# Kernel tuning notes

Hardware: AMD Instinct MI355X
Metric: run time of the kernel (lower is better)

Reference implementation:

```python
import jax, jax.numpy as jnp
import numpy as np

EPS = 1e-5  # RMSNorm epsilon


def rmsnorm(x, w):
    return x * jax.lax.rsqrt(jnp.mean(x * x, axis=-1, keepdims=True) + EPS) * w


def mamba_forward(u, in_proj_w, conv_w, conv_b, x_proj_w, dt_proj_w, dt_proj_b,
                  A_log, D_param, mamba_out_w):
    # u: (b, L, dm) -- canonical Mamba block (expand=2, d_state=16, d_conv=4)
    b, L, dm = u.shape
    di, ds = A_log.shape
    dtr = dt_proj_w.shape[1]
    xz = jnp.einsum('bld,ed->ble', u, in_proj_w)          # (b,L,2*di)
    x_, z = jnp.split(xz, 2, axis=-1)                     # each (b,L,di)
    # causal depthwise conv over the sequence axis
    dconv = conv_w.shape[-1]
    xc = jnp.transpose(x_, (0, 2, 1))                     # (b,di,L)
    xc = jnp.pad(xc, ((0, 0), (0, 0), (dconv - 1, 0)))
    xc = jax.lax.conv_general_dilated(xc, conv_w, window_strides=(1,), padding='VALID',
                                      dimension_numbers=('NCH', 'OIH', 'NCH'),
                                      feature_group_count=di)
    xc = xc + conv_b[None, :, None]
    x_ = jax.nn.silu(jnp.transpose(xc, (0, 2, 1)))        # (b,L,di)
    # input-dependent dt, B, C
    x_dbl = jnp.einsum('bld,ed->ble', x_, x_proj_w)       # (b,L,dtr+2*ds)
    dt, B, C = jnp.split(x_dbl, [dtr, dtr + ds], axis=-1)
    delta = jax.nn.softplus(jnp.einsum('blr,dr->bld', dt, dt_proj_w) + dt_proj_b)  # (b,L,di)
    A = -jnp.exp(A_log)                                   # (di,ds)

    def step(h, inp):
        d_t, B_t, C_t, x_t = inp                          # (b,di),(b,ds),(b,ds),(b,di)
        dA = jnp.exp(d_t[:, :, None] * A)                 # (b,di,ds)
        h = dA * h + (d_t * x_t)[:, :, None] * B_t[:, None, :]
        y = jnp.einsum('bds,bs->bd', h, C_t)
        return h, y

    xs = (jnp.moveaxis(delta, 1, 0), jnp.moveaxis(B, 1, 0),
          jnp.moveaxis(C, 1, 0), jnp.moveaxis(x_, 1, 0))
    h0 = jnp.zeros((b, di, ds), dtype=u.dtype)
    _, ys = jax.lax.scan(step, h0, xs)                    # ys: (L,b,di)
    y = jnp.moveaxis(ys, 0, 1) + x_ * D_param             # (b,L,di)
    y = y * jax.nn.silu(z)
    return jnp.einsum('bld,od->blo', y, mamba_out_w)      # (b,L,dm)


def conv1x1(W, bvec, t):
    # t: (b, cin, L) -> (b, cout, L)
    return jnp.einsum('oi,bit->bot', W, t) + bvec[None, :, None]


def reference(x, w_norm1, w_norm2, W_ip, b_ip, W_fp, b_fp, W_wp, b_wp, W_op, b_op,
              in_proj_w, conv_w, conv_b, x_proj_w, dt_proj_w, dt_proj_b,
              A_log, D_param, mamba_out_w):
    # x: (b, L, D) -- module's (b, c, l) with l == input_dim = D, c == seq = L
    residual = x
    xn = rmsnorm(x, w_norm1)                 # RMSNorm over last (input_dim) axis
    xt = jnp.transpose(xn, (0, 2, 1))        # 'b c l -> b l c' : (b, D, L)
    ssm = conv1x1(W_ip, b_ip, xt)            # (b, 2D, L)
    ssm = conv1x1(W_fp, b_fp, ssm)           # (b, 2D, L)
    u = jnp.transpose(ssm, (0, 2, 1))        # (b, L, 2D): seq=L, d_model=2D
    m = mamba_forward(u, in_proj_w, conv_w, conv_b, x_proj_w, dt_proj_w, dt_proj_b,
                      A_log, D_param, mamba_out_w)
    m = rmsnorm(m, w_norm2) + u              # PostNormMamba residual
    ssm = jnp.transpose(m, (0, 2, 1))        # (b, 2D, L)
    w = conv1x1(W_wp, b_wp, xt)              # (b, 2D, L)
    w = w * jax.nn.sigmoid(w)                # swish
    out = conv1x1(W_op, b_op, w * ssm)       # (b, D, L)
    return jnp.transpose(out, (0, 2, 1)) + residual


def setup_inputs():
    key = jax.random.key(0)
    ks = jax.random.split(key, 16)
    D, L, b = 64, 4096, 4
    dm, di, ds, dconv = 2 * D, 4 * D, 16, 4
    dtr = (dm + 15) // 16  # dt_rank = ceil(d_model/16) = 8

    def n(k, shape, fan_in):
        return jax.random.normal(k, shape, jnp.float32) * (1.0 / np.sqrt(fan_in))

    return {
        'x': jax.random.normal(ks[0], (b, L, D), jnp.float32),
        'w_norm1': jnp.ones((D,), jnp.float32),
        'w_norm2': jnp.ones((dm,), jnp.float32),
        'W_ip': n(ks[1], (2 * D, D), D), 'b_ip': jnp.zeros((2 * D,), jnp.float32),
        'W_fp': n(ks[2], (2 * D, 2 * D), 2 * D), 'b_fp': jnp.zeros((2 * D,), jnp.float32),
        'W_wp': n(ks[3], (2 * D, D), D), 'b_wp': jnp.zeros((2 * D,), jnp.float32),
        'W_op': n(ks[4], (D, 2 * D), 2 * D), 'b_op': jnp.zeros((D,), jnp.float32),
        'in_proj_w': n(ks[5], (2 * di, dm), dm),
        'conv_w': n(ks[6], (di, 1, dconv), dconv),
        'conv_b': jnp.zeros((di,), jnp.float32),
        'x_proj_w': n(ks[7], (dtr + 2 * ds, di), di),
        'dt_proj_w': n(ks[8], (di, dtr), dtr),
        'dt_proj_b': jnp.full((di,), float(np.log(np.expm1(0.01))), jnp.float32),
        'A_log': jnp.log(jnp.broadcast_to(jnp.arange(1, ds + 1, dtype=jnp.float32), (di, ds))),
        'D_param': jnp.ones((di,), jnp.float32),
        'mamba_out_w': n(ks[9], (dm, di), di),
    }
```

## Files before the change

kernel.cpp:

```cpp
#include <hip/hip_runtime.h>
#include <hip/hip_bf16.h>

typedef __hip_bfloat16 bf16;
typedef __attribute__((ext_vector_type(8))) short bf16x8;
typedef __attribute__((ext_vector_type(4))) float f32x4;
#define DEV __device__ __forceinline__

constexpr int SEQ  = 4096;
constexpr int NB   = 4;
constexpr int NTOK = NB * SEQ;
constexpr float EPS = 1e-5f;
constexpr int NCH = 64;
constexpr int NCHUNK = SEQ / NCH;
constexpr float LOG2E = 1.44269504f;

constexpr int OFF_WDT  = 0;
constexpr int OFF_WB   = 2048;
constexpr int WB_IP = 0;
constexpr int WB_WP = 8192;
constexpr int WB_FP = 16384;
constexpr int WB_PR = 32768;
constexpr int WB_MO = 98304;
constexpr int WB_OP = 131072;
constexpr int WB_XP = 139264;
constexpr int WB_TOT = 151552;
constexpr int OFF_XDBL = OFF_WB + WB_TOT / 2;
constexpr int OFF_R1   = OFF_XDBL + NTOK * 40;
constexpr int OFF_WSW  = OFF_R1   + 1048576;
constexpr int OFF_U    = OFF_WSW  + 1048576;
constexpr int OFF_R2   = OFF_U    + 1048576;
constexpr int OFF_SILUZ= OFF_R2   + 2097152;
constexpr int OFF_XC   = OFF_SILUZ+ 2097152;
constexpr int OFF_G    = OFF_XC   + 2097152;
constexpr int OFF_FLAG = OFF_G    + 2097152;

DEV float b2f(bf16 x) { return __bfloat162float(x); }
DEV bf16 f2b(float x) { return __float2bfloat16(x); }
DEV short shof(bf16 h) { short s; __builtin_memcpy(&s, &h, 2); return s; }
DEV float ldin(const void* p, int i, int f) {
  return f ? ((const float*)p)[i] : b2f(((const bf16*)p)[i]);
}
DEV unsigned pack2(float a, float b) {
  bf16 ha = f2b(a), hb = f2b(b);
  unsigned short ua, ub;
  __builtin_memcpy(&ua, &ha, 2); __builtin_memcpy(&ub, &hb, 2);
  return (unsigned)ua | ((unsigned)ub << 16);
}
DEV float lo16f(unsigned u) { return __int_as_float((int)(u << 16)); }
DEV float hi16f(unsigned u) { return __int_as_float((int)(u & 0xffff0000u)); }
template<int CTRL>
DEV float dpp_add(float v) {
  int r = __builtin_amdgcn_update_dpp(0, __float_as_int(v), CTRL, 0xF, 0xF, false);
  return v + __int_as_float(r);
}
DEV float exp2f_fast(float a) { return __builtin_amdgcn_exp2f(a); }
DEV float softplus(float a) {
  return (a > 20.f) ? a : __logf(1.f + exp2f_fast(a * LOG2E));
}
DEV float silu(float a) { return a / (1.f + __expf(-a)); }

DEV void cpw(int e, int base, int count, const void* __restrict__ src,
             bf16* __restrict__ wb, int f) {
  int r = e - base;
  if (r >= 0 && r < count) wb[base + r] = f2b(ldin(src, r, f));
}
__global__ __launch_bounds__(256) void prep_k(
    const void* __restrict__ w_ip, const void* __restrict__ w_wp, const void* __restrict__ w_fp,
    const void* __restrict__ w_pr, const void* __restrict__ w_mo, const void* __restrict__ w_op,
    const void* __restrict__ w_x,  const void* __restrict__ w_dt,
    const void* __restrict__ x, float* __restrict__ wsf, int* __restrict__ flagp)
{
  __shared__ int cnt;
  if (threadIdx.x == 0) cnt = 0;
  __syncthreads();
  {
    float v = b2f(((const bf16*)x)[threadIdx.x]);
    int ok = (v == v) && fabsf(v) > 1e-4f && fabsf(v) < 100.f;
    atomicAdd(&cnt, ok);
  }
  __syncthreads();
  int f = (cnt > 204) ? 0 : 1;
  if (blockIdx.x == 0 && threadIdx.x == 0) *flagp = f;

  int e = blockIdx.x * 256 + threadIdx.x;
  bf16* wb = (bf16*)(wsf + OFF_WB);
  cpw(e, WB_IP, 8192,  w_ip, wb, f);
  cpw(e, WB_WP, 8192,  w_wp, wb, f);
  cpw(e, WB_FP, 16384, w_fp, wb, f);
  cpw(e, WB_PR, 65536, w_pr, wb, f);
  cpw(e, WB_MO, 32768, w_mo, wb, f);
  cpw(e, WB_OP, 8192,  w_op, wb, f);
  {
    int r = e - WB_XP;
    if (r >= 0 && r < 12288) wb[WB_XP + r] = (r < 10240) ? f2b(ldin(w_x, r, f)) : f2b(0.f);
  }
  if (e < 2048) {
    int r = e >> 8, d = e & 255;
    wsf[OFF_WDT + e] = ldin(w_dt, d * 8 + r, f);
  }
}

__global__ __launch_bounds__(512) void fm_k(
    const void* __restrict__ x, const void* __restrict__ w1, const float* __restrict__ wsf,
    const void* __restrict__ b_ip, const void* __restrict__ b_wp, const void* __restrict__ b_fp,
    bf16* __restrict__ wsw, bf16* __restrict__ u, bf16* __restrict__ xpre,
    bf16* __restrict__ siluz, const int* __restrict__ flagp)
{
  __shared__ short xn[32 * 72];
  __shared__ short t1[32 * 136];
  __shared__ short ul[32 * 136];
  const int f = *flagp;
  const int tid = threadIdx.x;
  const int tok0 = blockIdx.x * 32;
  {
    const int token = tid >> 4, r = tid & 15;
    float v[4]; float ss = 0.f;
    #pragma unroll
    for (int k = 0; k < 4; ++k) {
      v[k] = ldin(x, (tok0 + token) * 64 + r * 4 + k, f);
      ss += v[k] * v[k];
    }
    ss += __shfl_xor(ss, 1, 16); ss += __shfl_xor(ss, 2, 16);
    ss += __shfl_xor(ss, 4, 16); ss += __shfl_xor(ss, 8, 16);
    float sc = rsqrtf(ss * (1.f / 64.f) + EPS);
    unsigned* dst = (unsigned*)xn + token * 36 + r * 2;
    #pragma unroll
    for (int k = 0; k < 2; ++k) {
      int i = r * 4 + k * 2;
      dst[k] = pack2(v[k*2] * sc * ldin(w1, i, f), v[k*2+1] * sc * ldin(w1, i + 1, f));
    }
  }
  __syncthreads();
  const int lane = tid & 63, m = lane & 15, q = lane >> 4;
  const int w = tid >> 6;
  {
    const int wt = w >> 2, ng = w & 3;
    const bf16* W = (const bf16*)(wsf + OFF_WB) + (wt ? WB_WP : WB_IP);
    const void* bia = wt ? b_wp : b_ip;
    bf16x8 a[2][2];
    #pragma unroll
    for (int mt = 0; mt < 2; ++mt)
      #pragma unroll
      for (int kk = 0; kk < 2; ++kk)
        a[mt][kk] = *(const bf16x8*)&xn[(mt * 16 + m) * 72 + kk * 32 + q * 8];
    #pragma unroll
    for (int nti = 0; nti < 2; ++nti) {
      int nt = ng * 2 + nti;
      int n = nt * 16 + m;
      f32x4 acc[2] = {{0,0,0,0},{0,0,0,0}};
      #pragma unroll
      for (int kk = 0; kk < 2; ++kk) {
        bf16x8 b = *(const bf16x8*)(W + (nt * 16 + m) * 64 + kk * 32 + q * 8);
        #pragma unroll
        for (int mt = 0; mt < 2; ++mt)
          acc[mt] = __builtin_amdgcn_mfma_f32_16x16x32_bf16(a[mt][kk], b, acc[mt], 0, 0, 0);
      }
      float bv = ldin(bia, n, f);
      #pragma unroll
      for (int mt = 0; mt < 2; ++mt)
        #pragma unroll
        for (int r = 0; r < 4; ++r) {
          float v = acc[mt][r] + bv;
          if (wt) wsw[(tok0 + mt * 16 + q * 4 + r) * 128 + n] = f2b(silu(v));
          else    t1[(mt * 16 + q * 4 + r) * 136 + n] = shof(f2b(v));
        }
    }
  }
  __syncthreads();
  {
    const bf16* WF = (const bf16*)(wsf + OFF_WB) + WB_FP;
    bf16x8 a[2][4];
    #pragma unroll
    for (int mt = 0; mt < 2; ++mt)
      #pragma unroll
      for (int kk = 0; kk < 4; ++kk)
        a[mt][kk] = *(const bf16x8*)&t1[(mt * 16 + m) * 136 + kk * 32 + q * 8];
    {
      int nt = w;
      int n = nt * 16 + m;
      f32x4 acc[2] = {{0,0,0,0},{0,0,0,0}};
      #pragma unroll
      for (int kk = 0; kk < 4; ++kk) {
        bf16x8 b = *(const bf16x8*)(WF + (nt * 16 + m) * 128 + kk * 32 + q * 8);
        #pragma unroll
        for (int mt = 0; mt < 2; ++mt)
          acc[mt] = __builtin_amdgcn_mfma_f32_16x16x32_bf16(a[mt][kk], b, acc[mt], 0, 0, 0);
      }
      float bv = ldin(b_fp, n, f);
      #pragma unroll
      for (int mt = 0; mt < 2; ++mt)
        #pragma unroll
        for (int r = 0; r < 4; ++r) {
          bf16 h = f2b(acc[mt][r] + bv);
          ul[(mt * 16 + q * 4 + r) * 136 + n] = shof(h);
          u[(tok0 + mt * 16 + q * 4 + r) * 128 + n] = h;
        }
    }
  }
  __syncthreads();
  {
    const bf16* WP = (const bf16*)(wsf + OFF_WB) + WB_PR;
    bf16x8 a[2][4];
    #pragma unroll
    for (int mt = 0; mt < 2; ++mt)
      #pragma unroll
      for (int kk = 0; kk < 4; ++kk)
        a[mt][kk] = *(const bf16x8*)&ul[(mt * 16 + m) * 136 + kk * 32 + q * 8];
    #pragma unroll
    for (int nti = 0; nti < 4; ++nti) {
      int nt = w * 4 + nti;
      int n = nt * 16 + m;
      f32x4 acc[2] = {{0,0,0,0},{0,0,0,0}};
      #pragma unroll
      for (int kk = 0; kk < 4; ++kk) {
        bf16x8 b = *(const bf16x8*)(WP + (nt * 16 + m) * 128 + kk * 32 + q * 8);
        #pragma unroll
        for (int mt = 0; mt < 2; ++mt)
          acc[mt] = __builtin_amdgcn_mfma_f32_16x16x32_bf16(a[mt][kk], b, acc[mt], 0, 0, 0);
      }
      #pragma unroll
      for (int mt = 0; mt < 2; ++mt)
        #pragma unroll
        for (int r = 0; r < 4; ++r) {
          int tok = tok0 + mt * 16 + q * 4 + r;
          if (n < 256) xpre[tok * 256 + n] = f2b(acc[mt][r]);
          else         siluz[tok * 256 + (n - 256)] = f2b(silu(acc[mt][r]));
        }
    }
  }
}

__global__ __launch_bounds__(256) void conv_k(
    const bf16* __restrict__ xpre, const void* __restrict__ cw, const void* __restrict__ cb,
    const float* __restrict__ wsf, bf16* __restrict__ xc, float* __restrict__ xdbl,
    const int* __restrict__ flagp)
{
  __shared__ short xh[35 * 256];
  __shared__ short cs[32 * 264];
  const int f = *flagp;
  const int tid = threadIdx.x;
  const int tok0 = blockIdx.x * 32;
  const bool seqstart = (tok0 & (SEQ - 1)) == 0;
  for (int c = tid; c < 1120; c += 256) {
    int e0 = c * 8;
    int tt = e0 >> 8, i = e0 & 255;
    int gtok = tok0 + tt - 3;
    uint4* dst = (uint4*)(xh + e0);
    if (gtok >= 0 && !(seqstart && tt < 3)) *dst = *(const uint4*)(xpre + gtok * 256 + i);
    else                                    *dst = make_uint4(0, 0, 0, 0);
  }
  __syncthreads();
  {
    const int ch0 = (tid & 63) * 4;
    const int t0 = (tid >> 6) * 8;
    float w4[4][4], cb4[4];
    #pragma unroll
    for (int c = 0; c < 4; ++c) {
      cb4[c] = ldin(cb, ch0 + c, f);
      #pragma unroll
      for (int k = 0; k < 4; ++k) w4[c][k] = ldin(cw, (ch0 + c) * 4 + k, f);
    }
    float win[11][4];
    #pragma unroll
    for (int r = 0; r < 11; ++r) {
      uint2 v = *(const uint2*)&xh[(t0 + r) * 256 + ch0];
      win[r][0] = lo16f(v.x); win[r][1] = hi16f(v.x);
      win[r][2] = lo16f(v.y); win[r][3] = hi16f(v.y);
    }
    #pragma unroll
    for (int t = 0; t < 8; ++t) {
      unsigned pk[2];
      #pragma unroll
      for (int cp = 0; cp < 2; ++cp) {
        float o[2];
        #pragma unroll
        for (int ci = 0; ci < 2; ++ci) {
          int c = cp * 2 + ci;
          float acc = cb4[c];
          #pragma unroll
          for (int k = 0; k < 4; ++k) acc = fmaf(win[t + k][c], w4[c][k], acc);
          o[ci] = silu(acc);
        }
        pk[cp] = pack2(o[0], o[1]);
      }
      uint2 pv = make_uint2(pk[0], pk[1]);
      *(uint2*)&cs[(t0 + t) * 264 + ch0] = pv;
      *(uint2*)(xc + (tok0 + t0 + t) * 256 + ch0) = pv;
    }
  }
  __syncthreads();
  const int w = tid >> 6;
  if (w < 2) {
    const bf16* Wx = (const bf16*)(wsf + OFF_WB) + WB_XP;
    const int lane = tid & 63, m = lane & 15, quad = lane >> 4;
    f32x4 acc[3] = {{0,0,0,0},{0,0,0,0},{0,0,0,0}};
    #pragma unroll
    for (int k0 = 0; k0 < 256; k0 += 32) {
      bf16x8 af = *(const bf16x8*)&cs[(w * 16 + m) * 264 + k0 + quad * 8];
      #pragma unroll
      for (int nt = 0; nt < 3; ++nt) {
        bf16x8 bfr = *(const bf16x8*)(Wx + (nt * 16 + m) * 256 + k0 + quad * 8);
        acc[nt] = __builtin_amdgcn_mfma_f32_16x16x32_bf16(af, bfr, acc[nt], 0, 0, 0);
      }
    }
    #pragma unroll
    for (int nt = 0; nt < 3; ++nt) {
      int n = nt * 16 + m;
      if (n < 40) {
        #pragma unroll
        for (int r = 0; r < 4; ++r)
          xdbl[(tok0 + w * 16 + quad * 4 + r) * 40 + n] = acc[nt][r];
      }
    }
  }
}

template<bool IS_C>
__global__ __launch_bounds__(256) void scan_k(
    const float* __restrict__ xdbl, const bf16* __restrict__ xc, const bf16* __restrict__ siluz,
    const void* __restrict__ A_log, const void* __restrict__ D_par, const void* __restrict__ dt_b,
    const float* __restrict__ WDT, float* __restrict__ summ, const float* __restrict__ hinit,
    bf16* __restrict__ g, const int* __restrict__ flagp)
{
  const int f = *flagp;
  const int tid = threadIdx.x;
  const int bb = blockIdx.x >> 4, dg = blockIdx.x & 15, c = blockIdx.y;
  const int dl = tid >> 4, s = tid & 15;
  const int j = s;
  const int d_loop = dg * 16 + dl;
  const int d_stg  = dg * 16 + j;
  const int tok_base = bb * SEQ + c * NCH;

  __shared__ float dt_l[NCH * 8];
  __shared__ float dx_l[NCH * 16 * 2];
  __shared__ float bc_l[IS_C ? NCH * 16 * 2 : NCH * 16];
  __shared__ float g_l[IS_C ? NCH * 16 : 1];

  const float Aval2 = -__expf(ldin(A_log, d_loop * 16 + s, f)) * LOG2E;
  const float Dp_stg = ldin(D_par, d_stg, f);
  const float dtb_j = ldin(dt_b, d_stg, f);
  float wdt[8];
  #pragma unroll
  for (int r = 0; r < 8; ++r) wdt[r] = WDT[r * 256 + d_stg];

  const int sidx = (blockIdx.x * NCHUNK + c) * 256 + tid;
  float h = IS_C ? hinit[sidx] : 0.f;
  float sdlt = 0.f;

  for (int e2 = tid * 4; e2 < NCH * 8; e2 += 1024)
    *(float4*)(dt_l + e2) = *(const float4*)(xdbl + (tok_base + (e2 >> 3)) * 40 + (e2 & 7));
  #pragma unroll
  for (int k = 0; k < 4; ++k) {
    int e = tid + k * 256;
    int t = e >> 4;
    int tok = tok_base + t;
    float B = xdbl[tok * 40 + 8 + j];
    if (IS_C) {
      bc_l[e * 2 + 0] = B;
      bc_l[e * 2 + 1] = xdbl[tok * 40 + 24 + j];
    } else bc_l[e] = B;
  }
  __syncthreads();
  #pragma unroll
  for (int k = 0; k < 4; ++k) {
    int e = tid + k * 256;
    int t = e >> 4;
    float a = dtb_j;
    #pragma unroll
    for (int r = 0; r < 8; ++r) a = fmaf(dt_l[t * 8 + r], wdt[r], a);
    float dlt = softplus(a);
    float xcv = b2f(xc[(tok_base + t) * 256 + d_stg]);
    *(float2*)(dx_l + e * 2) = make_float2(dlt, dlt * xcv);
  }
  __syncthreads();

  #pragma unroll 8
  for (int t = 0; t < NCH; ++t) {
    float2 dx = *(const float2*)(dx_l + (t * 16 + dl) * 2);
    float dA = exp2f_fast(dx.x * Aval2);
    if (!IS_C) sdlt += dx.x;
    if (IS_C) {
      float2 bc = *(const float2*)(bc_l + (t * 16 + s) * 2);
      h = fmaf(dA, h, dx.y * bc.x);
      float p = h * bc.y;
      p = dpp_add<0x121>(p);
      p = dpp_add<0x122>(p);
      p = dpp_add<0x124>(p);
      p = dpp_add<0x128>(p);
      if (s == 0) g_l[t * 16 + dl] = p;
    } else {
      h = fmaf(dA, h, dx.y * bc_l[t * 16 + s]);
    }
  }
  if (IS_C) {
    __syncthreads();
    #pragma unroll
    for (int k = 0; k < 4; ++k) {
      int e = tid + k * 256;
      int t = e >> 4;
      int tok = tok_base + t;
      float xcv = b2f(xc[tok * 256 + d_stg]);
      g[tok * 256 + d_stg] = f2b((g_l[e] + xcv * Dp_stg) * b2f(siluz[tok * 256 + d_stg]));
    }
  } else {
    *(float2*)(summ + sidx * 2) = make_float2(exp2f_fast(Aval2 * sdlt), h);
  }
}

__global__ __launch_bounds__(256) void scanB_k(const float* __restrict__ summ, float* __restrict__ hinit) {
  int bx = blockIdx.x, qq = threadIdx.x;
  float h = 0.f;
  for (int c0 = 0; c0 < NCHUNK; c0 += 16) {
    float2 sv[16];
    #pragma unroll
    for (int k = 0; k < 16; ++k)
      sv[k] = *(const float2*)(summ + ((bx * NCHUNK + c0 + k) * 256 + qq) * 2);
    #pragma unroll
    for (int k = 0; k < 16; ++k) {
      hinit[(bx * NCHUNK + c0 + k) * 256 + qq] = h;
      h = fmaf(sv[k].x, h, sv[k].y);
    }
  }
}

__global__ __launch_bounds__(512) void back_k(
    const bf16* __restrict__ g, const float* __restrict__ wsf, const void* __restrict__ w2,
    const bf16* __restrict__ u, const bf16* __restrict__ wsw, const void* __restrict__ b_op,
    const void* __restrict__ x, void* __restrict__ out, const int* __restrict__ flagp)
{
  __shared__ short ms[32 * 136];
  const int f = *flagp;
  const int tid = threadIdx.x;
  const int tok0 = blockIdx.x * 32;
  const int lane = tid & 63, m = lane & 15, q = lane >> 4;
  const int w = tid >> 6;
  const bf16* WM = (const bf16*)(wsf + OFF_WB) + WB_MO;
  const bf16* WO = (const bf16*)(wsf + OFF_WB) + WB_OP;
  {
    f32x4 acc[2] = {{0,0,0,0},{0,0,0,0}};
    #pragma unroll
    for (int kk = 0; kk < 8; ++kk) {
      bf16x8 a0 = *(const bf16x8*)(g + (tok0 + m) * 256 + kk * 32 + q * 8);
      bf16x8 a1 = *(const bf16x8*)(g + (tok0 + 16 + m) * 256 + kk * 32 + q * 8);
      int nt = w;
      bf16x8 b = *(const bf16x8*)(WM + (nt * 16 + m) * 256 + kk * 32 + q * 8);
      acc[0] = __builtin_amdgcn_mfma_f32_16x16x32_bf16(a0, b, acc[0], 0, 0, 0);
      acc[1] = __builtin_amdgcn_mfma_f32_16x16x32_bf16(a1, b, acc[1], 0, 0, 0);
    }
    {
      int n = w * 16 + m;
      #pragma unroll
      for (int mt = 0; mt < 2; ++mt)
        #pragma unroll
        for (int r = 0; r < 4; ++r)
          ms[(mt * 16 + q * 4 + r) * 136 + n] = shof(f2b(acc[mt][r]));
    }
  }
  __syncthreads();
  {
    const int token = tid >> 4, r = tid & 15;
    float mv[8]; float ss = 0.f;
    #pragma unroll
    for (int k = 0; k < 8; ++k) {
      mv[k] = b2f(((const bf16*)ms)[token * 136 + r * 8 + k]);
      ss += mv[k] * mv[k];
    }
    ss += __shfl_xor(ss, 1, 16); ss += __shfl_xor(ss, 2, 16);
    ss += __shfl_xor(ss, 4, 16); ss += __shfl_xor(ss, 8, 16);
    float sc = rsqrtf(ss * (1.f / 128.f) + EPS);
    #pragma unroll
    for (int k = 0; k < 8; ++k) {
      int i = r * 8 + k;
      int ga = (tok0 + token) * 128 + i;
      float v = mv[k] * sc * ldin(w2, i, f) + b2f(u[ga]);
      ms[token * 136 + i] = shof(f2b(v * b2f(wsw[ga])));
    }
  }
  __syncthreads();
  {
    const int mt = w >> 2, nt = w & 3;
    bf16x8 a[4];
    #pragma unroll
    for (int kk = 0; kk < 4; ++kk)
      a[kk] = *(const bf16x8*)&ms[(mt * 16 + m) * 136 + kk * 32 + q * 8];
    f32x4 acc = {0,0,0,0};
    #pragma unroll
    for (int kk = 0; kk < 4; ++kk) {
      bf16x8 b = *(const bf16x8*)(WO + (nt * 16 + m) * 128 + kk * 32 + q * 8);
      acc = __builtin_amdgcn_mfma_f32_16x16x32_bf16(a[kk], b, acc, 0, 0, 0);
    }
    int n = nt * 16 + m;
    float bv = ldin(b_op, n, f);
    #pragma unroll
    for (int r = 0; r < 4; ++r) {
      int token = tok0 + mt * 16 + q * 4 + r;
      float v = acc[r] + bv + ldin(x, token * 64 + n, f);
      if (f) ((float*)out)[token * 64 + n] = v;
      else   ((bf16*)out)[token * 64 + n] = f2b(v);
    }
  }
}

extern "C" void kernel_launch(void* const* d_in, const int* in_sizes, int n_in,
                              void* d_out, int out_size, void* d_ws, size_t ws_size,
                              hipStream_t stream) {
  (void)in_sizes; (void)n_in; (void)out_size; (void)ws_size;
  const void* x        = d_in[0];
  const void* w_norm1  = d_in[1];
  const void* w_norm2  = d_in[2];
  const void* W_ip     = d_in[3];
  const void* b_ip     = d_in[4];
  const void* W_fp     = d_in[5];
  const void* b_fp     = d_in[6];
  const void* W_wp     = d_in[7];
  const void* b_wp     = d_in[8];
  const void* W_op     = d_in[9];
  const void* b_op     = d_in[10];
  const void* in_proj  = d_in[11];
  const void* conv_w   = d_in[12];
  const void* conv_b   = d_in[13];
  const void* x_proj   = d_in[14];
  const void* dt_projw = d_in[15];
  const void* dt_projb = d_in[16];
  const void* A_log    = d_in[17];
  const void* D_par    = d_in[18];
  const void* mo_w     = d_in[19];

  float* wsf    = (float*)d_ws;
  float* xdbl   = wsf + OFF_XDBL;
  float* hin    = wsf + OFF_R1;
  bf16*  wsw_b  = (bf16*)(wsf + OFF_WSW);
  bf16*  u_b    = (bf16*)(wsf + OFF_U);
  bf16*  xpre_b = (bf16*)(wsf + OFF_R2);
  float* summ   = wsf + OFF_R2;
  bf16*  siluz_b= (bf16*)(wsf + OFF_SILUZ);
  bf16*  xc_b   = (bf16*)(wsf + OFF_XC);
  bf16*  g_b    = (bf16*)(wsf + OFF_G);
  int*   flagp  = (int*)(wsf + OFF_FLAG);

  prep_k<<<dim3(592), dim3(256), 0, stream>>>(W_ip, W_wp, W_fp, in_proj, mo_w, W_op,
                                              x_proj, dt_projw, x, wsf, flagp);
  fm_k<<<dim3(NTOK / 32), dim3(512), 0, stream>>>(x, w_norm1, wsf, b_ip, b_wp, b_fp,
                                                  wsw_b, u_b, xpre_b, siluz_b, flagp);
  conv_k<<<dim3(NTOK / 32), dim3(256), 0, stream>>>(xpre_b, conv_w, conv_b, wsf, xc_b, xdbl, flagp);
  scan_k<false><<<dim3(64, NCHUNK), dim3(256), 0, stream>>>(xdbl, xc_b, siluz_b, A_log, D_par,
                                                            dt_projb, wsf + OFF_WDT, summ, hin, g_b, flagp);
  scanB_k<<<dim3(64), dim3(256), 0, stream>>>(summ, hin);
  scan_k<true><<<dim3(64, NCHUNK), dim3(256), 0, stream>>>(xdbl, xc_b, siluz_b, A_log, D_par,
                                                           dt_projb, wsf + OFF_WDT, summ, hin, g_b, flagp);
  back_k<<<dim3(NTOK / 32), dim3(512), 0, stream>>>(g_b, wsf, w_norm2, u_b, wsw_b, b_op, x, d_out, flagp);
}
```

Before: 204.3 us.

## Give each scan thread four state elements and widen blocks to 64 channels

The chunked selective-scan kernels now assign four d_state elements per thread instead of one, and each block covers 64 channels instead of 16. This cuts the launch grid by a factor of four and replaces the 16-lane DPP reduction with a local 4-term FMA plus a 4-lane DPP reduction. The chunk is processed in two halves of 32 tokens to keep shared memory bounded. Loads of delta, B, C and xc are reused across more state elements and the global accesses widen to 64 contiguous channels, at the cost of fewer blocks, extra syncs and longer serial per-thread work.

```diff
diff --git a/kernel.cpp b/kernel.cpp
--- a/kernel.cpp
+++ b/kernel.cpp
@@ -324,86 +324,110 @@
 {
   const int f = *flagp;
   const int tid = threadIdx.x;
-  const int bb = blockIdx.x >> 4, dg = blockIdx.x & 15, c = blockIdx.y;
-  const int dl = tid >> 4, s = tid & 15;
-  const int j = s;
-  const int d_loop = dg * 16 + dl;
-  const int d_stg  = dg * 16 + j;
+  const int bb = blockIdx.x >> 2, dgsup = blockIdx.x & 3, c = blockIdx.y;
+  const int dgsub = tid >> 6, lane = tid & 63, dl = lane >> 2, squad = lane & 3;
+  const int dg = dgsup * 4 + dgsub;
+  const int bxOld = bb * 16 + dg;
+  const int d_comp = dg * 16 + dl;
+  const int bd = tid & 63;
+  const int d_stg = dgsup * 64 + bd;
+  const int bdc = dgsub * 16 + dl;
   const int tok_base = bb * SEQ + c * NCH;
 
   __shared__ float dt_l[NCH * 8];
-  __shared__ float dx_l[NCH * 16 * 2];
-  __shared__ float bc_l[IS_C ? NCH * 16 * 2 : NCH * 16];
-  __shared__ float g_l[IS_C ? NCH * 16 : 1];
-
-  const float Aval2 = -__expf(ldin(A_log, d_loop * 16 + s, f)) * LOG2E;
+  __shared__ float dx_l[32 * 64 * 2];
+  __shared__ float Bp[32 * 16];
+  __shared__ float Cp[IS_C ? 32 * 16 : 1];
+  __shared__ float g_l[IS_C ? 32 * 64 : 1];
+
+  float Aval2[4];
+  #pragma unroll
+  for (int j = 0; j < 4; ++j)
+    Aval2[j] = -__expf(ldin(A_log, d_comp * 16 + squad * 4 + j, f)) * LOG2E;
   const float Dp_stg = ldin(D_par, d_stg, f);
-  const float dtb_j = ldin(dt_b, d_stg, f);
+  const float dtb_stg = ldin(dt_b, d_stg, f);
   float wdt[8];
   #pragma unroll
   for (int r = 0; r < 8; ++r) wdt[r] = WDT[r * 256 + d_stg];
 
-  const int sidx = (blockIdx.x * NCHUNK + c) * 256 + tid;
-  float h = IS_C ? hinit[sidx] : 0.f;
+  float h[4] = {0.f, 0.f, 0.f, 0.f};
+  if (IS_C) {
+    float4 hv = *(const float4*)(hinit + (bxOld * NCHUNK + c) * 256 + dl * 16 + squad * 4);
+    h[0] = hv.x; h[1] = hv.y; h[2] = hv.z; h[3] = hv.w;
+  }
   float sdlt = 0.f;
 
-  for (int e2 = tid * 4; e2 < NCH * 8; e2 += 1024)
-    *(float4*)(dt_l + e2) = *(const float4*)(xdbl + (tok_base + (e2 >> 3)) * 40 + (e2 & 7));
-  #pragma unroll
-  for (int k = 0; k < 4; ++k) {
-    int e = tid + k * 256;
-    int t = e >> 4;
-    int tok = tok_base + t;
-    float B = xdbl[tok * 40 + 8 + j];
+  if (tid < 128)
+    *(float4*)(dt_l + tid * 4) = *(const float4*)(xdbl + (tok_base + (tid >> 1)) * 40 + (tid & 1) * 4);
+
+  #pragma unroll 1
+  for (int half = 0; half < 2; ++half) {
+    const int tb = half * 32;
+    __syncthreads();
+    #pragma unroll
+    for (int k = 0; k < 2; ++k) {
+      int e = tid + k * 256;
+      int tl = e >> 4, s = e & 15;
+      int tok = tok_base + tb + tl;
+      Bp[e] = xdbl[tok * 40 + 8 + s];
+      if (IS_C) Cp[e] = xdbl[tok * 40 + 24 + s];
+    }
+    #pragma unroll
+    for (int k = 0; k < 8; ++k) {
+      int tl = (tid >> 6) + k * 4;
+      int tok = tok_base + tb + tl;
+      const float* dtr = dt_l + (tb + tl) * 8;
+      float a = dtb_stg;
+      #pragma unroll
+      for (int r = 0; r < 8; ++r) a = fmaf(dtr[r], wdt[r], a);
+      float dlt = softplus(a);
+      float xcv = b2f(xc[tok * 256 + d_stg]);
+      *(float2*)(dx_l + (tl * 64 + bd) * 2) = make_float2(dlt, dlt * xcv);
+    }
+    __syncthreads();
+
+    #pragma unroll 8
+    for (int tl = 0; tl < 32; ++tl) {
+      float2 dx = *(const float2*)(dx_l + (tl * 64 + bdc) * 2);
+      float4 B4 = *(const float4*)(Bp + tl * 16 + squad * 4);
+      float Bv[4] = {B4.x, B4.y, B4.z, B4.w};
+      #pragma unroll
+      for (int j = 0; j < 4; ++j) {
+        float dA = exp2f_fast(dx.x * Aval2[j]);
+        h[j] = fmaf(dA, h[j], dx.y * Bv[j]);
+      }
+      if (IS_C) {
+        float4 C4 = *(const float4*)(Cp + tl * 16 + squad * 4);
+        float p = h[0] * C4.x;
+        p = fmaf(h[1], C4.y, p);
+        p = fmaf(h[2], C4.z, p);
+        p = fmaf(h[3], C4.w, p);
+        p = dpp_add<0xB1>(p);
+        p = dpp_add<0x4E>(p);
+        if (squad == 0) g_l[tl * 64 + bdc] = p;
+      } else {
+        sdlt += dx.x;
+      }
+    }
     if (IS_C) {
-      bc_l[e * 2 + 0] = B;
-      bc_l[e * 2 + 1] = xdbl[tok * 40 + 24 + j];
-    } else bc_l[e] = B;
-  }
-  __syncthreads();
-  #pragma unroll
-  for (int k = 0; k < 4; ++k) {
-    int e = tid + k * 256;
-    int t = e >> 4;
-    float a = dtb_j;
-    #pragma unroll
-    for (int r = 0; r < 8; ++r) a = fmaf(dt_l[t * 8 + r], wdt[r], a);
-    float dlt = softplus(a);
-    float xcv = b2f(xc[(tok_base + t) * 256 + d_stg]);
-    *(float2*)(dx_l + e * 2) = make_float2(dlt, dlt * xcv);
-  }
-  __syncthreads();
-
-  #pragma unroll 8
-  for (int t = 0; t < NCH; ++t) {
-    float2 dx = *(const float2*)(dx_l + (t * 16 + dl) * 2);
-    float dA = exp2f_fast(dx.x * Aval2);
-    if (!IS_C) sdlt += dx.x;
-    if (IS_C) {
-      float2 bc = *(const float2*)(bc_l + (t * 16 + s) * 2);
-      h = fmaf(dA, h, dx.y * bc.x);
-      float p = h * bc.y;
-      p = dpp_add<0x121>(p);
-      p = dpp_add<0x122>(p);
-      p = dpp_add<0x124>(p);
-      p = dpp_add<0x128>(p);
-      if (s == 0) g_l[t * 16 + dl] = p;
-    } else {
-      h = fmaf(dA, h, dx.y * bc_l[t * 16 + s]);
-    }
-  }
-  if (IS_C) {
-    __syncthreads();
-    #pragma unroll
-    for (int k = 0; k < 4; ++k) {
-      int e = tid + k * 256;
-      int t = e >> 4;
-      int tok = tok_base + t;
-      float xcv = b2f(xc[tok * 256 + d_stg]);
-      g[tok * 256 + d_stg] = f2b((g_l[e] + xcv * Dp_stg) * b2f(siluz[tok * 256 + d_stg]));
-    }
-  } else {
-    *(float2*)(summ + sidx * 2) = make_float2(exp2f_fast(Aval2 * sdlt), h);
+      __syncthreads();
+      #pragma unroll
+      for (int k = 0; k < 8; ++k) {
+        int tl = (tid >> 6) + k * 4;
+        int tok = tok_base + tb + tl;
+        float xcv = b2f(xc[tok * 256 + d_stg]);
+        g[tok * 256 + d_stg] =
+            f2b((g_l[tl * 64 + bd] + xcv * Dp_stg) * b2f(siluz[tok * 256 + d_stg]));
+      }
+    }
+  }
+
+  if (!IS_C) {
+    float* dst = summ + ((bxOld * NCHUNK + c) * 256 + dl * 16 + squad * 4) * 2;
+    *(float4*)(dst)     = make_float4(exp2f_fast(Aval2[0] * sdlt), h[0],
+                                      exp2f_fast(Aval2[1] * sdlt), h[1]);
+    *(float4*)(dst + 4) = make_float4(exp2f_fast(Aval2[2] * sdlt), h[2],
+                                      exp2f_fast(Aval2[3] * sdlt), h[3]);
   }
 }
 
@@ -543,10 +567,10 @@
   fm_k<<<dim3(NTOK / 32), dim3(512), 0, stream>>>(x, w_norm1, wsf, b_ip, b_wp, b_fp,
                                                   wsw_b, u_b, xpre_b, siluz_b, flagp);
   conv_k<<<dim3(NTOK / 32), dim3(256), 0, stream>>>(xpre_b, conv_w, conv_b, wsf, xc_b, xdbl, flagp);
-  scan_k<false><<<dim3(64, NCHUNK), dim3(256), 0, stream>>>(xdbl, xc_b, siluz_b, A_log, D_par,
+  scan_k<false><<<dim3(16, NCHUNK), dim3(256), 0, stream>>>(xdbl, xc_b, siluz_b, A_log, D_par,
                                                             dt_projb, wsf + OFF_WDT, summ, hin, g_b, flagp);
   scanB_k<<<dim3(64), dim3(256), 0, stream>>>(summ, hin);
-  scan_k<true><<<dim3(64, NCHUNK), dim3(256), 0, stream>>>(xdbl, xc_b, siluz_b, A_log, D_par,
+  scan_k<true><<<dim3(16, NCHUNK), dim3(256), 0, stream>>>(xdbl, xc_b, siluz_b, A_log, D_par,
                                                            dt_projb, wsf + OFF_WDT, summ, hin, g_b, flagp);
   back_k<<<dim3(NTOK / 32), dim3(512), 0, stream>>>(g_b, wsf, w_norm2, u_b, wsw_b, b_op, x, d_out, flagp);
 }
```

Result: faster. 197.5 us (-3.3%).
